# Optimization experiments

Measured on AMD Instinct MI355X. Metric: run time of the kernel, lower is better.

Reference implementation:

```python
import jax, jax.numpy as jnp
import numpy as np

NODE_TYPES = ["patient", "visit", "symptom", "procedure", "disease", "drug"]
N = {"patient": 20000, "visit": 100000, "symptom": 4000, "procedure": 8000,
     "disease": 10000, "drug": 4000}
D = 128          # embedding_dim == hidden_channels
N_LAYERS = 4     # conv1..conv4
# (src, dst) per relation; reverse edges included so every node type gets messages
REL = [("patient", "visit"), ("visit", "patient"),
       ("visit", "symptom"), ("symptom", "visit"),
       ("visit", "procedure"), ("procedure", "visit"),
       ("visit", "disease"), ("disease", "visit"),
       ("visit", "drug"), ("drug", "visit")]
E_FWD = {("patient", "visit"): 100000, ("visit", "symptom"): 300000,
         ("visit", "procedure"): 200000, ("visit", "disease"): 250000,
         ("visit", "drug"): 300000}
EI_NAMES = ["ei_pv", "ei_vp", "ei_vs", "ei_sv", "ei_vpr", "ei_prv",
            "ei_vd", "ei_dv", "ei_vdr", "ei_drv"]
E_LABEL = 200000


def setup_inputs() -> dict:
    key = jax.random.key(0)
    ks = iter(jax.random.split(key, 64))
    inp = {}
    for nt in NODE_TYPES:
        inp[f"node_id_{nt}"] = jnp.arange(N[nt], dtype=jnp.int32)
        inp[f"emb_{nt}"] = jax.random.normal(next(ks), (N[nt], D), jnp.float32)
    for name, (src, dst) in zip(EI_NAMES, REL):
        e = E_FWD.get((src, dst), E_FWD.get((dst, src)))
        row = jax.random.randint(next(ks), (e,), 0, N[src], dtype=jnp.int32)
        col = jax.random.randint(next(ks), (e,), 0, N[dst], dtype=jnp.int32)
        inp[name] = jnp.stack([row, col])
    R = len(REL)
    inp["W_l"] = jax.random.normal(next(ks), (N_LAYERS, R, D, D), jnp.float32) * 0.05
    inp["b_l"] = jnp.zeros((N_LAYERS, R, D), jnp.float32)
    inp["W_r"] = jax.random.normal(next(ks), (N_LAYERS, R, D, D), jnp.float32) * 0.05
    inp["cls_w1"] = jax.random.normal(next(ks), (2 * D, D), jnp.float32) * 0.05
    inp["cls_b1"] = jnp.zeros((D,), jnp.float32)
    inp["cls_w2"] = jax.random.normal(next(ks), (D, 1), jnp.float32) * 0.05
    inp["cls_b2"] = jnp.zeros((1,), jnp.float32)
    row = jax.random.randint(next(ks), (E_LABEL,), 0, N["visit"], dtype=jnp.int32)
    col = jax.random.randint(next(ks), (E_LABEL,), 0, N["drug"], dtype=jnp.int32)
    inp["edge_label_index"] = jnp.stack([row, col])
    inp["edge_label"] = jax.random.bernoulli(next(ks), 0.5, (E_LABEL,)).astype(jnp.float32)
    return inp


def _hetero_sage_layer(x, eis, Wl, bl, Wr):
    # to_hetero semantics: out[dst] = sum over edge types (src,rel,dst) of
    #   SAGEConv_rel: lin_l(mean_j x[src][j]) + lin_r(x[dst])   (PyG defaults)
    out = {nt: jnp.zeros_like(v) for nt, v in x.items()}
    for r, (src, dst) in enumerate(REL):
        ei = eis[r]
        n_dst = x[dst].shape[0]
        msg = jax.ops.segment_sum(x[src][ei[0]], ei[1], num_segments=n_dst)
        deg = jax.ops.segment_sum(jnp.ones((ei.shape[1],), x[src].dtype), ei[1],
                                  num_segments=n_dst)
        mean = msg / jnp.maximum(deg, 1.0)[:, None]  # empty segments stay 0 as in PyG
        out[dst] = out[dst] + mean @ Wl[r] + bl[r] + x[dst] @ Wr[r]
    return out


def reference(node_id_patient, node_id_visit, node_id_symptom, node_id_procedure,
              node_id_disease, node_id_drug,
              emb_patient, emb_visit, emb_symptom, emb_procedure, emb_disease, emb_drug,
              ei_pv, ei_vp, ei_vs, ei_sv, ei_vpr, ei_prv, ei_vd, ei_dv, ei_vdr, ei_drv,
              W_l, b_l, W_r, cls_w1, cls_b1, cls_w2, cls_b2,
              edge_label_index, edge_label):
    x = {"patient": emb_patient[node_id_patient],
         "visit": emb_visit[node_id_visit],
         "symptom": emb_symptom[node_id_symptom],
         "procedure": emb_procedure[node_id_procedure],
         "disease": emb_disease[node_id_disease],
         "drug": emb_drug[node_id_drug]}
    eis = [ei_pv, ei_vp, ei_vs, ei_sv, ei_vpr, ei_prv, ei_vd, ei_dv, ei_vdr, ei_drv]
    for l in range(N_LAYERS):
        x = _hetero_sage_layer(x, eis, W_l[l], b_l[l], W_r[l])
        if l < N_LAYERS - 1:  # relu after conv1..conv3 only; dropout is eval-mode identity
            x = {k: jax.nn.relu(v) for k, v in x.items()}
    # Classifier: gather visit/drug node features per labeled edge, concat, MLP
    zv = x["visit"][edge_label_index[0]]
    zd = x["drug"][edge_label_index[1]]
    h = jax.nn.relu(jnp.concatenate([zv, zd], axis=-1) @ cls_w1 + cls_b1)
    pred = (h @ cls_w2 + cls_b2).reshape(-1)
    # BCE with logits: softplus(z) - z*y, mean-reduced
    loss = jnp.mean(jax.nn.softplus(pred) - pred * edge_label)
    return loss, pred
```

## Files before the change

kernel.cpp:

```cpp
#include <hip/hip_runtime.h>
#include <cmath>


typedef _Float16 f16x8 __attribute__((ext_vector_type(8)));
typedef _Float16 f16x4 __attribute__((ext_vector_type(4)));
typedef float f32x4 __attribute__((ext_vector_type(4)));

#define NREL 10
#define NCOUNTS 546000
#define NEDGES  2300000
#define NVISIT  100000
#define PLW 546816
#define WT_ELEMS (4 * PLW + 67584)
#define XELEMS 18688000UL
#define SELEMS 5888000UL
#define NBKT 873
#define BCAP 5120

struct GatherMeta { const float* emb[6]; const int* nid[6]; int rows[6]; int off[6]; };
struct AggMeta { const int* rp[5]; _Float16* meanH[5]; _Float16* meanL[5]; int M[5]; };
struct VAggMeta { const int* rp[5]; const _Float16* Y[5]; };
struct BkMeta {
  const int* ei[NREL]; int E[NREL]; int cbc[NREL]; int ndst[NREL];
  int sh[NREL]; int bb[NREL]; int nb[NREL];
};
struct MTask {
  const _Float16* AH0; const _Float16* AL0;
  const _Float16* AH1; const _Float16* AL1;
  const _Float16* W;
  const float* bias;
  _Float16* outH; _Float16* outL;
  int M, blkOff, K, relu;
};
struct MMeta { MTask t[6]; int nTasks; };

__global__ __launch_bounds__(256) void conv0(GatherMeta g, _Float16* __restrict__ H,
                                             _Float16* __restrict__ L) {
  int t = blockIdx.y;
  int i = blockIdx.x * 256 + threadIdx.x;
  if (i >= g.rows[t] * 16) return;
  int row = i >> 4, q = i & 15;
  int s = g.nid[t][row];
  const float* p = g.emb[t] + (size_t)s * 128 + q * 8;
  float4 v0 = *(const float4*)p;
  float4 v1 = *(const float4*)(p + 4);
  float v[8] = {v0.x, v0.y, v0.z, v0.w, v1.x, v1.y, v1.z, v1.w};
  f16x8 h, l;
  #pragma unroll
  for (int j = 0; j < 8; ++j) {
    h[j] = (_Float16)v[j];
    l[j] = (_Float16)(v[j] - (float)h[j]);
  }
  size_t o = (size_t)(g.off[t] + row) * 128 + q * 8;
  *(f16x8*)(H + o) = h;
  *(f16x8*)(L + o) = l;
}

__global__ __launch_bounds__(256) void bkt_p1(BkMeta bm, int* __restrict__ bcur,
                                              int* __restrict__ bdata) {
  __shared__ int cnt[128];
  __shared__ int base[128];
  __shared__ unsigned short rnk[4096];
  int r = blockIdx.y;
  int E = bm.E[r], sh = bm.sh[r], bb = bm.bb[r], nb = bm.nb[r];
  int tid = threadIdx.x;
  if (tid < 128) cnt[tid] = 0;
  __syncthreads();
  int e0 = blockIdx.x * 4096;
  if (e0 >= E) return;
  const int* dstp = bm.ei[r] + E;
  const int* srcp = bm.ei[r];
  #pragma unroll
  for (int i = 0; i < 16; ++i) {
    int e = e0 + i * 256 + tid;
    if (e < E) {
      int b = dstp[e] >> sh;
      rnk[i * 256 + tid] = (unsigned short)atomicAdd(&cnt[b], 1);
    }
  }
  __syncthreads();
  if (tid < nb && cnt[tid] > 0) base[tid] = atomicAdd(&bcur[bb + tid], cnt[tid]);
  __syncthreads();
  #pragma unroll
  for (int i = 0; i < 16; ++i) {
    int e = e0 + i * 256 + tid;
    if (e < E) {
      int d = dstp[e];
      int b = d >> sh;
      int pos = base[b] + (int)rnk[i * 256 + tid];
      if (pos < BCAP)
        bdata[(size_t)(bb + b) * BCAP + pos] = ((d & ((1 << sh) - 1)) << 17) | srcp[e];
    }
  }
}

__global__ __launch_bounds__(256) void bkt_p2a(BkMeta bm, const int* __restrict__ bcur,
                                               const int* __restrict__ bdata,
                                               int* __restrict__ counts) {
  __shared__ int hist[2048];
  int g = blockIdx.x;
  int r = 0;
  #pragma unroll
  for (int i = 1; i < NREL; ++i) if (g >= bm.bb[i]) r = i;
  int lb = g - bm.bb[r];
  int sh = bm.sh[r], dpb = 1 << sh;
  int tid = threadIdx.x;
  for (int d = tid; d < dpb; d += 256) hist[d] = 0;
  __syncthreads();
  int cnt = bcur[g]; if (cnt > BCAP) cnt = BCAP;
  const int* bd = bdata + (size_t)g * BCAP;
  for (int i = tid; i < cnt; i += 256) atomicAdd(&hist[((unsigned)bd[i]) >> 17], 1);
  __syncthreads();
  int dBase = lb << sh;
  int dMax = bm.ndst[r] - dBase; if (dMax > dpb) dMax = dpb;
  for (int d = tid; d < dMax; d += 256) counts[bm.cbc[r] + dBase + d] = hist[d];
}

__global__ __launch_bounds__(1024) void scan1(const int* __restrict__ counts,
                                              int* __restrict__ partials) {
  __shared__ int s[1024];
  int i = blockIdx.x * 1024 + threadIdx.x;
  s[threadIdx.x] = (i < NCOUNTS) ? counts[i] : 0;
  __syncthreads();
  for (int off = 512; off > 0; off >>= 1) {
    if (threadIdx.x < off) s[threadIdx.x] += s[threadIdx.x + off];
    __syncthreads();
  }
  if (threadIdx.x == 0) partials[blockIdx.x] = s[0];
}

__global__ __launch_bounds__(1024) void scan2(int* __restrict__ partials, int nb) {
  __shared__ int s[1024];
  int t = threadIdx.x;
  int v = (t < nb) ? partials[t] : 0;
  s[t] = v;
  __syncthreads();
  for (int off = 1; off < 1024; off <<= 1) {
    int add = (t >= off) ? s[t - off] : 0;
    __syncthreads();
    s[t] += add;
    __syncthreads();
  }
  if (t < nb) partials[t] = s[t] - v;
}

__global__ __launch_bounds__(1024) void scan3(const int* __restrict__ counts,
                                              int* __restrict__ prefix,
                                              const int* __restrict__ partials) {
  __shared__ int s[1024];
  int t = threadIdx.x;
  int i = blockIdx.x * 1024 + t;
  int v = (i < NCOUNTS) ? counts[i] : 0;
  s[t] = v;
  __syncthreads();
  for (int off = 1; off < 1024; off <<= 1) {
    int add = (t >= off) ? s[t - off] : 0;
    __syncthreads();
    s[t] += add;
    __syncthreads();
  }
  int P = partials[blockIdx.x] + s[t] - v;
  if (i < NCOUNTS) prefix[i] = P;
  if (blockIdx.x == 0 && t == 0) prefix[NCOUNTS] = NEDGES;
}

__global__ __launch_bounds__(256) void bkt_p2b(BkMeta bm, const int* __restrict__ bcur,
                                               const int* __restrict__ bdata,
                                               const int* __restrict__ prefix,
                                               int* __restrict__ esrc) {
  __shared__ int pk[BCAP];
  __shared__ int srt[BCAP];
  __shared__ int cur[2048];
  __shared__ int part[256];
  __shared__ int baseSh;
  int g = blockIdx.x;
  int r = 0;
  #pragma unroll
  for (int i = 1; i < NREL; ++i) if (g >= bm.bb[i]) r = i;
  int lb = g - bm.bb[r];
  int sh = bm.sh[r], dpb = 1 << sh;
  int tid = threadIdx.x;
  int cnt = bcur[g]; if (cnt > BCAP) cnt = BCAP;
  const int* bd = bdata + (size_t)g * BCAP;
  for (int d = tid; d < dpb; d += 256) cur[d] = 0;
  for (int i = tid; i < cnt; i += 256) pk[i] = bd[i];
  __syncthreads();
  for (int i = tid; i < cnt; i += 256) atomicAdd(&cur[((unsigned)pk[i]) >> 17], 1);
  __syncthreads();
  int seg = (dpb + 255) >> 8;
  int s = 0;
  int b0 = tid * seg;
  for (int j = 0; j < seg; ++j) {
    int idx = b0 + j;
    if (idx < dpb) { int v = cur[idx]; cur[idx] = s; s += v; }
  }
  part[tid] = s;
  __syncthreads();
  for (int off = 1; off < 256; off <<= 1) {
    int add = (tid >= off) ? part[tid - off] : 0;
    __syncthreads();
    part[tid] += add;
    __syncthreads();
  }
  int myoff = part[tid] - s;
  for (int j = 0; j < seg; ++j) {
    int idx = b0 + j;
    if (idx < dpb) cur[idx] += myoff;
  }
  if (tid == 0) baseSh = prefix[bm.cbc[r] + (lb << sh)];
  __syncthreads();
  for (int i = tid; i < cnt; i += 256) {
    int p = pk[i];
    int pos = atomicAdd(&cur[((unsigned)p) >> 17], 1);
    srt[pos] = p & 0x1FFFF;
  }
  __syncthreads();
  int base = baseSh;
  for (int i = tid; i < cnt; i += 256) esrc[base + i] = srt[i];
}

__global__ __launch_bounds__(256) void prep_split(
    const float* __restrict__ W_l, const float* __restrict__ b_l,
    const float* __restrict__ W_r, const float* __restrict__ cw1,
    _Float16* __restrict__ Wt, float* __restrict__ visitSumB) {
  const int visitRel[5] = {0, 3, 5, 7, 9};
  const int inRel[5] = {1, 2, 4, 6, 8};
  int gid = blockIdx.x * 256 + threadIdx.x;
  if (gid < 1048576) {
    int l = gid >> 18, o = gid & 262143;
    float val; size_t base; int n, k, Kpad;
    if (o < 163840) {
      int t = o >> 15, e = o & 32767;
      k = e >> 7; n = e & 127; Kpad = 264;
      int r = inRel[t];
      val = (k < 128) ? W_l[(size_t)(l * 10 + r) * 16384 + k * 128 + n]
                      : W_r[(size_t)(l * 10 + r) * 16384 + (k - 128) * 128 + n];
      base = (size_t)l * PLW + t * 67584;
    } else if (o < 245760) {
      int q = (o - 163840) >> 14, e = (o - 163840) & 16383;
      k = e >> 7; n = e & 127; Kpad = 136;
      val = W_l[(size_t)(l * 10 + visitRel[q]) * 16384 + k * 128 + n];
      base = (size_t)l * PLW + 337920 + q * 34816;
    } else {
      int e = o - 245760;
      k = e >> 7; n = e & 127; Kpad = 136;
      val = 0.f;
      #pragma unroll
      for (int q = 0; q < 5; ++q)
        val += W_r[(size_t)(l * 10 + visitRel[q]) * 16384 + k * 128 + n];
      base = (size_t)l * PLW + 512000;
    }
    _Float16 h = (_Float16)val;
    _Float16 lo = (_Float16)(val - (float)h);
    Wt[base + (size_t)n * Kpad + k] = h;
    Wt[base + (size_t)(128 + n) * Kpad + k] = lo;
  } else if (gid < 1081344) {
    int e = gid - 1048576;
    int k = e >> 7, n = e & 127;
    float val = cw1[(size_t)k * 128 + n];
    _Float16 h = (_Float16)val;
    _Float16 lo = (_Float16)(val - (float)h);
    size_t base = (size_t)4 * PLW;
    Wt[base + (size_t)n * 264 + k] = h;
    Wt[base + (size_t)(128 + n) * 264 + k] = lo;
  } else if (gid < 1081856) {
    int e = gid - 1081344;
    int l = e >> 7, c = e & 127;
    float val = 0.f;
    #pragma unroll
    for (int q = 0; q < 5; ++q) val += b_l[(l * 10 + visitRel[q]) * 128 + c];
    visitSumB[e] = val;
  }
}

__global__ __launch_bounds__(256) void agg_small(AggMeta m,
                                                 const _Float16* __restrict__ xvH,
                                                 const int* __restrict__ esrc) {
  int t = blockIdx.y;
  int row = blockIdx.x * 16 + (threadIdx.x >> 4);
  if (row >= m.M[t]) return;
  int q = threadIdx.x & 15;
  const int* rp = m.rp[t];
  int e0 = rp[row], e1 = rp[row + 1];
  float a[8];
  #pragma unroll
  for (int j = 0; j < 8; ++j) a[j] = 0.f;
  int e = e0;
  for (; e + 4 <= e1; e += 4) {
    int s0 = esrc[e], s1 = esrc[e + 1], s2 = esrc[e + 2], s3 = esrc[e + 3];
    f16x8 v0 = *(const f16x8*)(xvH + (size_t)s0 * 128 + q * 8);
    f16x8 v1 = *(const f16x8*)(xvH + (size_t)s1 * 128 + q * 8);
    f16x8 v2 = *(const f16x8*)(xvH + (size_t)s2 * 128 + q * 8);
    f16x8 v3 = *(const f16x8*)(xvH + (size_t)s3 * 128 + q * 8);
    #pragma unroll
    for (int j = 0; j < 8; ++j)
      a[j] += ((float)v0[j] + (float)v1[j]) + ((float)v2[j] + (float)v3[j]);
  }
  for (; e < e1; ++e) {
    int s = esrc[e];
    f16x8 v = *(const f16x8*)(xvH + (size_t)s * 128 + q * 8);
    #pragma unroll
    for (int j = 0; j < 8; ++j) a[j] += (float)v[j];
  }
  float inv = (e1 > e0) ? 1.f / (float)(e1 - e0) : 0.f;
  f16x8 h, l;
  #pragma unroll
  for (int j = 0; j < 8; ++j) {
    float v = a[j] * inv;
    h[j] = (_Float16)v;
    l[j] = (_Float16)(v - (float)h[j]);
  }
  size_t o = (size_t)row * 128 + q * 8;
  *(f16x8*)(m.meanH[t] + o) = h;
  *(f16x8*)(m.meanL[t] + o) = l;
}

__global__ __launch_bounds__(256) void agg_visit(VAggMeta va, const int* __restrict__ esrc,
                                                 _Float16* __restrict__ xvH,
                                                 _Float16* __restrict__ xvL, int doRelu) {
  int row = blockIdx.x * 16 + (threadIdx.x >> 4);
  if (row >= NVISIT) return;
  int q = threadIdx.x & 15;
  size_t o = (size_t)row * 128 + q * 8;
  f16x8 h0 = *(f16x8*)(xvH + o);
  f16x8 l0 = *(f16x8*)(xvL + o);
  float a[8];
  #pragma unroll
  for (int j = 0; j < 8; ++j) a[j] = (float)h0[j] + (float)l0[j];
  #pragma unroll
  for (int r = 0; r < 5; ++r) {
    int e0 = va.rp[r][row], e1 = va.rp[r][row + 1];
    if (e1 > e0) {
      const _Float16* Y = va.Y[r];
      float s[8];
      #pragma unroll
      for (int j = 0; j < 8; ++j) s[j] = 0.f;
      int e = e0;
      for (; e + 4 <= e1; e += 4) {
        int s0 = esrc[e], s1 = esrc[e + 1], s2 = esrc[e + 2], s3 = esrc[e + 3];
        f16x8 v0 = *(const f16x8*)(Y + (size_t)s0 * 128 + q * 8);
        f16x8 v1 = *(const f16x8*)(Y + (size_t)s1 * 128 + q * 8);
        f16x8 v2 = *(const f16x8*)(Y + (size_t)s2 * 128 + q * 8);
        f16x8 v3 = *(const f16x8*)(Y + (size_t)s3 * 128 + q * 8);
        #pragma unroll
        for (int j = 0; j < 8; ++j)
          s[j] += ((float)v0[j] + (float)v1[j]) + ((float)v2[j] + (float)v3[j]);
      }
      for (; e < e1; ++e) {
        int si = esrc[e];
        f16x8 v = *(const f16x8*)(Y + (size_t)si * 128 + q * 8);
        #pragma unroll
        for (int j = 0; j < 8; ++j) s[j] += (float)v[j];
      }
      float inv = 1.f / (float)(e1 - e0);
      #pragma unroll
      for (int j = 0; j < 8; ++j) a[j] += s[j] * inv;
    }
  }
  f16x8 h, l;
  #pragma unroll
  for (int j = 0; j < 8; ++j) {
    float v = doRelu ? fmaxf(a[j], 0.f) : a[j];
    h[j] = (_Float16)v;
    l[j] = (_Float16)(v - (float)h[j]);
  }
  *(f16x8*)(xvH + o) = h;
  *(f16x8*)(xvL + o) = l;
}

__global__ __launch_bounds__(256, 2) void mgemm(MMeta mm) {
  int b = blockIdx.x;
  int ti = 0;
  for (int i = 1; i < mm.nTasks; ++i) if (b >= mm.t[i].blkOff) ti = i;
  MTask tk = mm.t[ti];
  int blockRow = (b - tk.blkOff) * 128;
  int Kpad = tk.K + 8;

  __shared__ _Float16 Ash[2][128][72];
  int tid = threadIdx.x;
  int wave = tid >> 6, lane = tid & 63;
  int quad = lane >> 4, lm = lane & 15;
  int wr = wave >> 1, wc = wave & 1;

  f32x4 acc[4][4];
  #pragma unroll
  for (int i = 0; i < 4; ++i)
    #pragma unroll
    for (int j = 0; j < 4; ++j) acc[i][j] = (f32x4){0.f, 0.f, 0.f, 0.f};

  const _Float16* wrowH[4];
  const _Float16* wrowL[4];
  #pragma unroll
  for (int nt = 0; nt < 4; ++nt) {
    int n = wc * 64 + nt * 16 + lm;
    wrowH[nt] = tk.W + (size_t)n * Kpad;
    wrowL[nt] = tk.W + (size_t)(128 + n) * Kpad;
  }

  int sr = tid >> 1, sk = (tid & 1) * 32;
  int gr = blockRow + sr; if (gr >= tk.M) gr = tk.M - 1;
  for (int k0 = 0; k0 < tk.K; k0 += 64) {
    const _Float16* AH = (k0 < 128) ? tk.AH0 : tk.AH1;
    const _Float16* AL = (k0 < 128) ? tk.AL0 : tk.AL1;
    size_t abase = (size_t)gr * 128 + (k0 & 127) + sk;
    #pragma unroll
    for (int c = 0; c < 4; ++c) {
      *(f16x8*)&Ash[0][sr][sk + c * 8] = *(const f16x8*)(AH + abase + c * 8);
      *(f16x8*)&Ash[1][sr][sk + c * 8] = *(const f16x8*)(AL + abase + c * 8);
    }
    __syncthreads();
    #pragma unroll
    for (int ks = 0; ks < 64; ks += 32) {
      int kf = k0 + ks + quad * 8;
      f16x8 bh[4], bl[4];
      #pragma unroll
      for (int nt = 0; nt < 4; ++nt) {
        bh[nt] = *(const f16x8*)(wrowH[nt] + kf);
        bl[nt] = *(const f16x8*)(wrowL[nt] + kf);
      }
      #pragma unroll
      for (int mt = 0; mt < 4; ++mt) {
        int r = wr * 64 + mt * 16 + lm;
        f16x8 ah = *(const f16x8*)&Ash[0][r][ks + quad * 8];
        f16x8 al = *(const f16x8*)&Ash[1][r][ks + quad * 8];
        #pragma unroll
        for (int nt = 0; nt < 4; ++nt) {
          acc[mt][nt] = __builtin_amdgcn_mfma_f32_16x16x32_f16(ah, bh[nt], acc[mt][nt], 0, 0, 0);
          acc[mt][nt] = __builtin_amdgcn_mfma_f32_16x16x32_f16(ah, bl[nt], acc[mt][nt], 0, 0, 0);
          acc[mt][nt] = __builtin_amdgcn_mfma_f32_16x16x32_f16(al, bh[nt], acc[mt][nt], 0, 0, 0);
        }
      }
    }
    __syncthreads();
  }

  float bv[4];
  #pragma unroll
  for (int nt = 0; nt < 4; ++nt)
    bv[nt] = tk.bias ? tk.bias[wc * 64 + nt * 16 + lm] : 0.f;
  #pragma unroll
  for (int mt = 0; mt < 4; ++mt) {
    #pragma unroll
    for (int i = 0; i < 4; ++i) {
      int grow = blockRow + wr * 64 + mt * 16 + quad * 4 + i;
      if (grow >= tk.M) continue;
      size_t ob = (size_t)grow * 128 + wc * 64 + lm;
      #pragma unroll
      for (int nt = 0; nt < 4; ++nt) {
        float v = acc[mt][nt][i] + bv[nt];
        if (tk.relu) v = fmaxf(v, 0.f);
        _Float16 h = (_Float16)v;
        tk.outH[ob + nt * 16] = h;
        if (tk.outL) tk.outL[ob + nt * 16] = (_Float16)(v - (float)h);
      }
    }
  }
}

__global__ __launch_bounds__(256, 2) void mgemm_cls(
    const _Float16* __restrict__ xv16, const _Float16* __restrict__ xd16,
    const int* __restrict__ eli, const _Float16* __restrict__ W,
    const float* __restrict__ b1, const float* __restrict__ w2,
    const float* __restrict__ b2, const float* __restrict__ y,
    float* __restrict__ lossOut, float* __restrict__ pred, int M) {
  __shared__ _Float16 Ash[128][72];
  __shared__ int idxA[128];
  __shared__ int idxB[128];
  __shared__ float predPart[128];
  __shared__ float redL[128];
  int tid = threadIdx.x;
  int wave = tid >> 6, lane = tid & 63;
  int quad = lane >> 4, lm = lane & 15;
  int wr = wave >> 1, wc = wave & 1;
  int blockRow = blockIdx.x * 128;
  if (tid < 128) {
    int gr = blockRow + tid;
    idxA[tid] = (gr < M) ? eli[gr] : 0;
  } else {
    int t2 = tid - 128;
    int gr = blockRow + t2;
    idxB[t2] = (gr < M) ? eli[M + gr] : 0;
  }
  f32x4 acc[4][4];
  #pragma unroll
  for (int i = 0; i < 4; ++i)
    #pragma unroll
    for (int j = 0; j < 4; ++j) acc[i][j] = (f32x4){0.f, 0.f, 0.f, 0.f};

  const _Float16* wrowH[4];
  const _Float16* wrowL[4];
  #pragma unroll
  for (int nt = 0; nt < 4; ++nt) {
    int n = wc * 64 + nt * 16 + lm;
    wrowH[nt] = W + (size_t)n * 264;
    wrowL[nt] = W + (size_t)(128 + n) * 264;
  }
  __syncthreads();

  int sr = tid >> 1, sk = (tid & 1) * 32;
  for (int k0 = 0; k0 < 256; k0 += 64) {
    const _Float16* base = (k0 < 128) ? xv16 : xd16;
    int srcRow = (k0 < 128) ? idxA[sr] : idxB[sr];
    const _Float16* p = base + (size_t)srcRow * 128 + (k0 & 127) + sk;
    #pragma unroll
    for (int c = 0; c < 4; ++c)
      *(f16x8*)&Ash[sr][sk + c * 8] = *(const f16x8*)(p + c * 8);
    __syncthreads();
    #pragma unroll
    for (int ks = 0; ks < 64; ks += 32) {
      int kf = k0 + ks + quad * 8;
      f16x8 bh[4], bl[4];
      #pragma unroll
      for (int nt = 0; nt < 4; ++nt) {
        bh[nt] = *(const f16x8*)(wrowH[nt] + kf);
        bl[nt] = *(const f16x8*)(wrowL[nt] + kf);
      }
      #pragma unroll
      for (int mt = 0; mt < 4; ++mt) {
        int r = wr * 64 + mt * 16 + lm;
        f16x8 ah = *(const f16x8*)&Ash[r][ks + quad * 8];
        #pragma unroll
        for (int nt = 0; nt < 4; ++nt) {
          acc[mt][nt] = __builtin_amdgcn_mfma_f32_16x16x32_f16(ah, bh[nt], acc[mt][nt], 0, 0, 0);
          acc[mt][nt] = __builtin_amdgcn_mfma_f32_16x16x32_f16(ah, bl[nt], acc[mt][nt], 0, 0, 0);
        }
      }
    }
    __syncthreads();
  }

  float b1v[4], w2v[4];
  #pragma unroll
  for (int nt = 0; nt < 4; ++nt) {
    int col = wc * 64 + nt * 16 + lm;
    b1v[nt] = b1[col];
    w2v[nt] = w2[col];
  }
  float rowp[4][4];
  #pragma unroll
  for (int mt = 0; mt < 4; ++mt)
    #pragma unroll
    for (int i = 0; i < 4; ++i) {
      float p = 0.f;
      #pragma unroll
      for (int nt = 0; nt < 4; ++nt)
        p += fmaxf(acc[mt][nt][i] + b1v[nt], 0.f) * w2v[nt];
      p += __shfl_xor(p, 1);
      p += __shfl_xor(p, 2);
      p += __shfl_xor(p, 4);
      p += __shfl_xor(p, 8);
      rowp[mt][i] = p;
    }
  if (wc == 0 && lm == 0) {
    #pragma unroll
    for (int mt = 0; mt < 4; ++mt)
      #pragma unroll
      for (int i = 0; i < 4; ++i)
        predPart[wr * 64 + mt * 16 + quad * 4 + i] = rowp[mt][i];
  }
  __syncthreads();
  if (wc == 1 && lm == 0) {
    #pragma unroll
    for (int mt = 0; mt < 4; ++mt)
      #pragma unroll
      for (int i = 0; i < 4; ++i)
        predPart[wr * 64 + mt * 16 + quad * 4 + i] += rowp[mt][i];
  }
  __syncthreads();
  if (tid < 128) {
    int gr = blockRow + tid;
    float lv = 0.f;
    if (gr < M) {
      float z = predPart[tid] + b2[0];
      pred[gr] = z;
      lv = fmaxf(z, 0.f) + log1pf(expf(-fabsf(z))) - z * y[gr];
    }
    redL[tid] = lv;
  }
  __syncthreads();
  if (tid == 0) {
    float s = 0.f;
    for (int i = 0; i < 128; ++i) s += redL[i];
    atomicAdd(lossOut, s * (1.0f / 200000.0f));
  }
}

extern "C" void kernel_launch(void* const* d_in, const int* in_sizes, int n_in,
                              void* d_out, int out_size, void* d_ws, size_t ws_size,
                              hipStream_t stream) {
  static const int kRows[6] = {20000, 100000, 4000, 8000, 10000, 4000};
  static const int kOff[6]  = {0, 20000, 120000, 124000, 132000, 142000};
  static const int kSmallT[5]   = {0, 2, 3, 4, 5};
  static const int kInRel[5]    = {1, 2, 4, 6, 8};
  static const int kCbcIn[5]    = {100000, 120000, 224000, 332000, 442000};
  static const int kCbcVisit[5] = {0, 124000, 232000, 342000, 446000};
  static const int kYOff[5]     = {0, 20000, 24000, 32000, 42000};
  static const int kBOff[5]     = {0, 157, 189, 252, 331};
  static const int kCbcA[NREL]  = {0, 100000, 120000, 124000, 224000,
                                   232000, 332000, 342000, 442000, 446000};
  static const int kEhA[NREL]   = {100000, 100000, 300000, 300000, 200000,
                                   200000, 250000, 250000, 300000, 300000};
  static const int kNdst[NREL]  = {100000, 20000, 4000, 100000, 8000,
                                   100000, 10000, 100000, 4000, 100000};
  static const int kSh[NREL]    = {11, 9, 5, 10, 7, 10, 7, 10, 5, 10};
  static const int kNB[NREL]    = {49, 40, 125, 98, 63, 98, 79, 98, 125, 98};
  static const int kBB[NREL]    = {0, 49, 89, 214, 312, 375, 473, 552, 650, 775};

  const float* W_l = (const float*)d_in[22];
  const float* b_l = (const float*)d_in[23];
  const float* W_r = (const float*)d_in[24];
  const float* cw1 = (const float*)d_in[25];
  const float* cb1 = (const float*)d_in[26];
  const float* cw2 = (const float*)d_in[27];
  const float* cb2 = (const float*)d_in[28];
  const int* eli = (const int*)d_in[29];
  const float* ylab = (const float*)d_in[30];

  _Float16* H = (_Float16*)d_ws;
  _Float16* L = H + XELEMS;
  _Float16* meanH = L + XELEMS;
  _Float16* meanL = meanH + SELEMS;
  _Float16* YH = meanL + SELEMS;
  _Float16* Wt = YH + SELEMS;
  int* prefix = (int*)(Wt + WT_ELEMS);
  int* counts = prefix + 546004;
  int* esrc = counts + NCOUNTS;
  int* partials = esrc + NEDGES;
  float* visitSumB = (float*)(partials + 1024);
  int* bcur = (int*)(visitSumB + 512);
  int* bdata = bcur + 1024;

  BkMeta bm;
  for (int r = 0; r < NREL; ++r) {
    bm.ei[r] = (const int*)d_in[12 + r];
    bm.E[r] = kEhA[r];
    bm.cbc[r] = kCbcA[r];
    bm.ndst[r] = kNdst[r];
    bm.sh[r] = kSh[r];
    bm.bb[r] = kBB[r];
    bm.nb[r] = kNB[r];
  }

  hipMemsetAsync(bcur, 0, NBKT * sizeof(int), stream);
  hipMemsetAsync(d_out, 0, sizeof(float), stream);

  prep_split<<<(1081856 + 255) / 256, 256, 0, stream>>>(W_l, b_l, W_r, cw1, Wt, visitSumB);

  GatherMeta gm;
  for (int t = 0; t < 6; ++t) {
    gm.nid[t] = (const int*)d_in[2 * t];
    gm.emb[t] = (const float*)d_in[2 * t + 1];
    gm.rows[t] = kRows[t];
    gm.off[t] = kOff[t];
  }
  conv0<<<dim3(6250, 6), 256, 0, stream>>>(gm, H, L);

  bkt_p1<<<dim3(74, NREL), 256, 0, stream>>>(bm, bcur, bdata);
  bkt_p2a<<<dim3(NBKT), 256, 0, stream>>>(bm, bcur, bdata, counts);
  scan1<<<534, 1024, 0, stream>>>(counts, partials);
  scan2<<<1, 1024, 0, stream>>>(partials, 534);
  scan3<<<534, 1024, 0, stream>>>(counts, prefix, partials);
  bkt_p2b<<<dim3(NBKT), 256, 0, stream>>>(bm, bcur, bdata, prefix, esrc);

  _Float16* xvH = H + (size_t)kOff[1] * 128;
  _Float16* xvL = L + (size_t)kOff[1] * 128;

  for (int l = 0; l < 4; ++l) {
    int doRelu = (l < 3);
    int last = (l == 3);
    _Float16* LW = Wt + (size_t)l * PLW;

    AggMeta am;
    if (!last) {
      for (int t = 0; t < 5; ++t) {
        am.rp[t] = prefix + kCbcIn[t];
        am.meanH[t] = meanH + (size_t)kYOff[t] * 128;
        am.meanL[t] = meanL + (size_t)kYOff[t] * 128;
        am.M[t] = kRows[kSmallT[t]];
      }
      agg_small<<<dim3(1250, 5), 256, 0, stream>>>(am, xvH, esrc);
    } else {
      am.rp[0] = prefix + kCbcIn[4];
      am.meanH[0] = meanH + (size_t)kYOff[4] * 128;
      am.meanL[0] = meanL + (size_t)kYOff[4] * 128;
      am.M[0] = 4000;
      agg_small<<<dim3(250, 1), 256, 0, stream>>>(am, xvH, esrc);
    }

    MMeta m2;
    m2.nTasks = 6;
    for (int q = 0; q < 5; ++q) {
      size_t so = (size_t)kOff[kSmallT[q]] * 128;
      m2.t[q].AH0 = H + so; m2.t[q].AL0 = L + so;
      m2.t[q].AH1 = nullptr; m2.t[q].AL1 = nullptr;
      m2.t[q].W = LW + 337920 + (size_t)q * 34816;
      m2.t[q].bias = nullptr;
      m2.t[q].outH = YH + (size_t)kYOff[q] * 128;
      m2.t[q].outL = nullptr;
      m2.t[q].M = kRows[kSmallT[q]];
      m2.t[q].blkOff = kBOff[q];
      m2.t[q].K = 128;
      m2.t[q].relu = 0;
    }
    m2.t[5].AH0 = xvH; m2.t[5].AL0 = xvL;
    m2.t[5].AH1 = nullptr; m2.t[5].AL1 = nullptr;
    m2.t[5].W = LW + 512000;
    m2.t[5].bias = visitSumB + l * 128;
    m2.t[5].outH = xvH; m2.t[5].outL = xvL;
    m2.t[5].M = NVISIT;
    m2.t[5].blkOff = 363;
    m2.t[5].K = 128;
    m2.t[5].relu = 0;
    mgemm<<<dim3(363 + 782), 256, 0, stream>>>(m2);

    MMeta m1;
    if (!last) {
      m1.nTasks = 5;
      for (int t = 0; t < 5; ++t) {
        size_t mo = (size_t)kYOff[t] * 128;
        size_t so = (size_t)kOff[kSmallT[t]] * 128;
        m1.t[t].AH0 = meanH + mo; m1.t[t].AL0 = meanL + mo;
        m1.t[t].AH1 = H + so;     m1.t[t].AL1 = L + so;
        m1.t[t].W = LW + (size_t)t * 67584;
        m1.t[t].bias = b_l + (size_t)(l * 10 + kInRel[t]) * 128;
        m1.t[t].outH = H + so;    m1.t[t].outL = L + so;
        m1.t[t].M = kRows[kSmallT[t]];
        m1.t[t].blkOff = kBOff[t];
        m1.t[t].K = 256;
        m1.t[t].relu = doRelu;
      }
      mgemm<<<dim3(363), 256, 0, stream>>>(m1);
    } else {
      size_t mo = (size_t)kYOff[4] * 128;
      size_t so = (size_t)kOff[5] * 128;
      m1.nTasks = 1;
      m1.t[0].AH0 = meanH + mo; m1.t[0].AL0 = meanL + mo;
      m1.t[0].AH1 = H + so;     m1.t[0].AL1 = L + so;
      m1.t[0].W = LW + (size_t)4 * 67584;
      m1.t[0].bias = b_l + (size_t)(l * 10 + kInRel[4]) * 128;
      m1.t[0].outH = H + so;    m1.t[0].outL = L + so;
      m1.t[0].M = 4000;
      m1.t[0].blkOff = 0;
      m1.t[0].K = 256;
      m1.t[0].relu = 0;
      mgemm<<<dim3(32), 256, 0, stream>>>(m1);
    }

    VAggMeta va;
    for (int q = 0; q < 5; ++q) {
      va.rp[q] = prefix + kCbcVisit[q];
      va.Y[q] = YH + (size_t)kYOff[q] * 128;
    }
    agg_visit<<<dim3(6250), 256, 0, stream>>>(va, esrc, xvH, xvL, doRelu);
  }

  const int ML = 200000;
  mgemm_cls<<<dim3((ML + 127) / 128), 256, 0, stream>>>(
      xvH, H + (size_t)kOff[5] * 128, eli, Wt + (size_t)4 * PLW, cb1, cw2, cb2, ylab,
      (float*)d_out, (float*)d_out + 1, ML);
}
```

Before: 983.7 us.

## Merge five visit-relation CSR lists into one weighted edge list

Adds a one-time merge kernel that builds a single CSR per visit row, concatenating the five incoming relations with a global source index and a precomputed 1/deg weight packed as int2. agg_visit then walks one edge list with a 4-way unrolled loop instead of five short per-relation loops. This is meant to cut per-relation prefix loads and tail-loop overhead and to improve load-level parallelism for low-degree rows. The cost is one extra kernel, larger 8-byte edge entries, and reuse of the counts and bdata buffers as scratch for the merged arrays.

```diff
diff --git a/kernel.cpp b/kernel.cpp
--- a/kernel.cpp
+++ b/kernel.cpp
@@ -10,6 +10,7 @@
 #define NCOUNTS 546000
 #define NEDGES  2300000
 #define NVISIT  100000
+#define NVEDGES 1150000
 #define PLW 546816
 #define WT_ELEMS (4 * PLW + 67584)
 #define XELEMS 18688000UL
@@ -19,7 +20,6 @@
 
 struct GatherMeta { const float* emb[6]; const int* nid[6]; int rows[6]; int off[6]; };
 struct AggMeta { const int* rp[5]; _Float16* meanH[5]; _Float16* meanL[5]; int M[5]; };
-struct VAggMeta { const int* rp[5]; const _Float16* Y[5]; };
 struct BkMeta {
   const int* ei[NREL]; int E[NREL]; int cbc[NREL]; int ndst[NREL];
   int sh[NREL]; int bb[NREL]; int nb[NREL];
@@ -217,6 +217,41 @@
   __syncthreads();
   int base = baseSh;
   for (int i = tid; i < cnt; i += 256) esrc[base + i] = srt[i];
+}
+
+__global__ __launch_bounds__(256) void merge_visit(const int* __restrict__ prefix,
+                                                   const int* __restrict__ esrc,
+                                                   int* __restrict__ mprefix,
+                                                   int2* __restrict__ mesrc) {
+  const int cbc[5]  = {0, 124000, 232000, 342000, 446000};
+  const int yoff[5] = {0, 20000, 24000, 32000, 42000};
+  int v = blockIdx.x * 256 + threadIdx.x;
+  if (v >= NVISIT) return;
+  int e0[5], e1[5];
+  int base = 0;
+  #pragma unroll
+  for (int q = 0; q < 5; ++q) {
+    e0[q] = prefix[cbc[q] + v];
+    e1[q] = prefix[cbc[q] + v + 1];
+    base += e0[q] - prefix[cbc[q]];
+  }
+  mprefix[v] = base;
+  if (v == NVISIT - 1) {
+    int t = base;
+    #pragma unroll
+    for (int q = 0; q < 5; ++q) t += e1[q] - e0[q];
+    mprefix[NVISIT] = t;
+  }
+  int pos = base;
+  #pragma unroll
+  for (int q = 0; q < 5; ++q) {
+    int d = e1[q] - e0[q];
+    if (d > 0) {
+      int wb = __float_as_int(1.f / (float)d);
+      for (int e = e0[q]; e < e1[q]; ++e)
+        mesrc[pos++] = make_int2(yoff[q] + esrc[e], wb);
+    }
+  }
 }
 
 __global__ __launch_bounds__(256) void prep_split(
@@ -315,7 +350,9 @@
   *(f16x8*)(m.meanL[t] + o) = l;
 }
 
-__global__ __launch_bounds__(256) void agg_visit(VAggMeta va, const int* __restrict__ esrc,
+__global__ __launch_bounds__(256) void agg_visit(const int* __restrict__ mprefix,
+                                                 const int2* __restrict__ mesrc,
+                                                 const _Float16* __restrict__ YH,
                                                  _Float16* __restrict__ xvH,
                                                  _Float16* __restrict__ xvL, int doRelu) {
   int row = blockIdx.x * 16 + (threadIdx.x >> 4);
@@ -327,35 +364,27 @@
   float a[8];
   #pragma unroll
   for (int j = 0; j < 8; ++j) a[j] = (float)h0[j] + (float)l0[j];
-  #pragma unroll
-  for (int r = 0; r < 5; ++r) {
-    int e0 = va.rp[r][row], e1 = va.rp[r][row + 1];
-    if (e1 > e0) {
-      const _Float16* Y = va.Y[r];
-      float s[8];
-      #pragma unroll
-      for (int j = 0; j < 8; ++j) s[j] = 0.f;
-      int e = e0;
-      for (; e + 4 <= e1; e += 4) {
-        int s0 = esrc[e], s1 = esrc[e + 1], s2 = esrc[e + 2], s3 = esrc[e + 3];
-        f16x8 v0 = *(const f16x8*)(Y + (size_t)s0 * 128 + q * 8);
-        f16x8 v1 = *(const f16x8*)(Y + (size_t)s1 * 128 + q * 8);
-        f16x8 v2 = *(const f16x8*)(Y + (size_t)s2 * 128 + q * 8);
-        f16x8 v3 = *(const f16x8*)(Y + (size_t)s3 * 128 + q * 8);
-        #pragma unroll
-        for (int j = 0; j < 8; ++j)
-          s[j] += ((float)v0[j] + (float)v1[j]) + ((float)v2[j] + (float)v3[j]);
-      }
-      for (; e < e1; ++e) {
-        int si = esrc[e];
-        f16x8 v = *(const f16x8*)(Y + (size_t)si * 128 + q * 8);
-        #pragma unroll
-        for (int j = 0; j < 8; ++j) s[j] += (float)v[j];
-      }
-      float inv = 1.f / (float)(e1 - e0);
-      #pragma unroll
-      for (int j = 0; j < 8; ++j) a[j] += s[j] * inv;
-    }
+  int e0 = mprefix[row], e1 = mprefix[row + 1];
+  int e = e0;
+  for (; e + 4 <= e1; e += 4) {
+    int2 p0 = mesrc[e], p1 = mesrc[e + 1], p2 = mesrc[e + 2], p3 = mesrc[e + 3];
+    f16x8 v0 = *(const f16x8*)(YH + (size_t)p0.x * 128 + q * 8);
+    f16x8 v1 = *(const f16x8*)(YH + (size_t)p1.x * 128 + q * 8);
+    f16x8 v2 = *(const f16x8*)(YH + (size_t)p2.x * 128 + q * 8);
+    f16x8 v3 = *(const f16x8*)(YH + (size_t)p3.x * 128 + q * 8);
+    float w0 = __int_as_float(p0.y), w1 = __int_as_float(p1.y);
+    float w2 = __int_as_float(p2.y), w3 = __int_as_float(p3.y);
+    #pragma unroll
+    for (int j = 0; j < 8; ++j)
+      a[j] += (w0 * (float)v0[j] + w1 * (float)v1[j]) +
+              (w2 * (float)v2[j] + w3 * (float)v3[j]);
+  }
+  for (; e < e1; ++e) {
+    int2 p = mesrc[e];
+    f16x8 v = *(const f16x8*)(YH + (size_t)p.x * 128 + q * 8);
+    float w = __int_as_float(p.y);
+    #pragma unroll
+    for (int j = 0; j < 8; ++j) a[j] += w * (float)v[j];
   }
   f16x8 h, l;
   #pragma unroll
@@ -593,7 +622,6 @@
   static const int kSmallT[5]   = {0, 2, 3, 4, 5};
   static const int kInRel[5]    = {1, 2, 4, 6, 8};
   static const int kCbcIn[5]    = {100000, 120000, 224000, 332000, 442000};
-  static const int kCbcVisit[5] = {0, 124000, 232000, 342000, 446000};
   static const int kYOff[5]     = {0, 20000, 24000, 32000, 42000};
   static const int kBOff[5]     = {0, 157, 189, 252, 331};
   static const int kCbcA[NREL]  = {0, 100000, 120000, 124000, 224000,
@@ -630,6 +658,9 @@
   int* bcur = (int*)(visitSumB + 512);
   int* bdata = bcur + 1024;
 
+  int* mprefix = counts;
+  int2* mesrc = (int2*)bdata;
+
   BkMeta bm;
   for (int r = 0; r < NREL; ++r) {
     bm.ei[r] = (const int*)d_in[12 + r];
@@ -661,6 +692,7 @@
   scan2<<<1, 1024, 0, stream>>>(partials, 534);
   scan3<<<534, 1024, 0, stream>>>(counts, prefix, partials);
   bkt_p2b<<<dim3(NBKT), 256, 0, stream>>>(bm, bcur, bdata, prefix, esrc);
+  merge_visit<<<dim3((NVISIT + 255) / 256), 256, 0, stream>>>(prefix, esrc, mprefix, mesrc);
 
   _Float16* xvH = H + (size_t)kOff[1] * 128;
   _Float16* xvL = L + (size_t)kOff[1] * 128;
@@ -746,12 +778,7 @@
       mgemm<<<dim3(32), 256, 0, stream>>>(m1);
     }
 
-    VAggMeta va;
-    for (int q = 0; q < 5; ++q) {
-      va.rp[q] = prefix + kCbcVisit[q];
-      va.Y[q] = YH + (size_t)kYOff[q] * 128;
-    }
-    agg_visit<<<dim3(6250), 256, 0, stream>>>(va, esrc, xvH, xvL, doRelu);
+    agg_visit<<<dim3(6250), 256, 0, stream>>>(mprefix, mesrc, YH, xvH, xvL, doRelu);
   }
 
   const int ML = 200000;
```

New measurement: 925.2 us. 1.06x faster.
